# Performance work log

Hardware: AMD Instinct MI355X
Metric: run time of the kernel (lower is better)

Reference implementation:

```python
import jax, jax.numpy as jnp
import numpy as np
import math

D_SINGLE, D_PAIR, H, PQ, PV = 384, 128, 12, 4, 8
DH = D_SINGLE // H
OUT_DIM = H * DH + H * PV * 4 + H * D_PAIR


def setup_inputs() -> dict:
    key = jax.random.key(0)
    ks = jax.random.split(key, 24)
    B, L = 1, 512
    inp = {
        'single': jax.random.normal(ks[0], (B, L, D_SINGLE), jnp.float32),
        'pair': jax.random.normal(ks[1], (B, L, L, D_PAIR), jnp.float32),
        'rot_mats': jax.random.normal(ks[2], (B, L, 3, 3), jnp.float32),
        'trans': jax.random.normal(ks[3], (B, L, 3), jnp.float32),
        'mask': jnp.ones((B, L), jnp.float32),
        'ln_w': jnp.ones((D_SINGLE,), jnp.float32),
        'ln_b': jnp.zeros((D_SINGLE,), jnp.float32),
        'Wq': jax.random.normal(ks[4], (D_SINGLE, H * DH), jnp.float32) * 0.02,
        'bq': jnp.zeros((H * DH,), jnp.float32),
        'Wk': jax.random.normal(ks[5], (D_SINGLE, H * DH), jnp.float32) * 0.02,
        'bk': jnp.zeros((H * DH,), jnp.float32),
        'Wv': jax.random.normal(ks[6], (D_SINGLE, H * DH), jnp.float32) * 0.02,
        'bv': jnp.zeros((H * DH,), jnp.float32),
        'Wqp': jax.random.normal(ks[7], (D_SINGLE, H * PQ * 3), jnp.float32) * 0.02,
        'bqp': jnp.zeros((H * PQ * 3,), jnp.float32),
        'Wkp': jax.random.normal(ks[8], (D_SINGLE, H * PQ * 3), jnp.float32) * 0.02,
        'bkp': jnp.zeros((H * PQ * 3,), jnp.float32),
        'Wvp': jax.random.normal(ks[9], (D_SINGLE, H * PV * 3), jnp.float32) * 0.02,
        'bvp': jnp.zeros((H * PV * 3,), jnp.float32),
        'Wpb': jax.random.normal(ks[10], (D_PAIR, H), jnp.float32) * 0.02,
        'bpb': jnp.zeros((H,), jnp.float32),
        'Wo': jax.random.normal(ks[11], (OUT_DIM, D_SINGLE), jnp.float32) * 0.02,
        'bo': jnp.zeros((D_SINGLE,), jnp.float32),
        'w_c': jnp.asarray(1.0 / math.sqrt(3.0), jnp.float32),
        'w_l': jnp.asarray(1.0 / 3.0, jnp.float32),
        'gamma_h': jnp.ones((H,), jnp.float32),
    }
    return inp


def _layer_norm(x, w, b, eps=1e-5):
    mu = jnp.mean(x, axis=-1, keepdims=True)
    var = jnp.mean((x - mu) ** 2, axis=-1, keepdims=True)
    return (x - mu) * jax.lax.rsqrt(var + eps) * w + b


def reference(single, pair, rot_mats, trans, mask, ln_w, ln_b, Wq, bq, Wk, bk, Wv, bv,
              Wqp, bqp, Wkp, bkp, Wvp, bvp, Wpb, bpb, Wo, bo, w_c, w_l, gamma_h):
    B, L, _ = single.shape
    sn = _layer_norm(single, ln_w, ln_b)
    q = (sn @ Wq + bq).reshape(B, L, H, DH)
    k = (sn @ Wk + bk).reshape(B, L, H, DH)
    v = (sn @ Wv + bv).reshape(B, L, H, DH)
    qp = (sn @ Wqp + bqp).reshape(B, L, H, PQ, 3)
    kp = (sn @ Wkp + bkp).reshape(B, L, H, PQ, 3)
    vp = (sn @ Wvp + bvp).reshape(B, L, H, PV, 3)

    t = trans[:, :, None, None, :]  # [B,L,1,1,3]
    qg = jnp.einsum('blij,blhpj->blhpi', rot_mats, qp) + t
    kg = jnp.einsum('blij,blhpj->blhpi', rot_mats, kp) + t
    vg = jnp.einsum('blij,blhpj->blhpi', rot_mats, vp) + t

    # sequence logits [B,H,L,L]
    seq_logits = jnp.einsum('bihd,bjhd->bhij', q, k) * w_c / math.sqrt(DH)

    # geometric logits: pairwise point distances [B,H,L,L]
    q_pts = jnp.transpose(qg, (0, 2, 1, 3, 4))  # [B,H,L,PQ,3]
    k_pts = jnp.transpose(kg, (0, 2, 1, 3, 4))
    diff = q_pts[:, :, :, None] - k_pts[:, :, None]  # [B,H,L,L,PQ,3]
    dist_sq = jnp.sum(diff ** 2, axis=-1)            # [B,H,L,L,PQ]
    geo_logits = -0.5 * jnp.sum(dist_sq, axis=-1) * gamma_h[None, :, None, None] * w_l

    pair_bias = jnp.transpose(pair @ Wpb + bpb, (0, 3, 1, 2))  # [B,H,L,L]
    logits = seq_logits + geo_logits + pair_bias

    mask_2d = (mask[:, :, None] * mask[:, None, :])[:, None]  # [B,1,L,L]
    logits = jnp.where(mask_2d > 0, logits, jnp.float32(-1e9))
    attn = jax.nn.softmax(logits, axis=-1)  # [B,H,L,L]

    # sequence aggregation -> [B,L,H,DH]
    seq_out = jnp.einsum('bhij,bjhd->bihd', attn, v).reshape(B, L, H * DH)

    # point aggregation -> local frame features
    pts_out = jnp.einsum('bhij,bjhpd->bihpd', attn, vg)  # [B,L,H,PV,3]
    pts_local = jnp.einsum('blji,blhpj->blhpi', rot_mats, pts_out - t)
    pts_norm = jnp.linalg.norm(pts_local, axis=-1, keepdims=True)
    pts_feat = jnp.concatenate([pts_norm, pts_local], axis=-1).reshape(B, L, H * PV * 4)

    # pair aggregation -> [B,L,H*D_PAIR]
    pair_out = jnp.einsum('bhij,bijd->bihd', attn, pair).reshape(B, L, H * D_PAIR)

    combined = jnp.concatenate([seq_out, pts_feat, pair_out], axis=-1)
    return combined @ Wo + bo
```

## Files before the change

### kernel.cpp

```cpp
#include <hip/hip_runtime.h>
#include <math.h>

#define LQ    512
#define DS    384
#define DPAIR 128
#define NH    12
#define NPP   1792
#define FE2   64
#define TJC   64
#define NC    8

typedef unsigned short u16;
typedef unsigned int   u32;
typedef __attribute__((ext_vector_type(8))) short bf16x8;
typedef __attribute__((ext_vector_type(4))) float f32x4;

__device__ inline u16 bf16_rne(float x) {
  u32 u = __float_as_uint(x);
  u32 r = (u + 0x7FFFu + ((u >> 16) & 1u)) >> 16;
  return (u16)r;
}
__device__ inline void split_bf16(float x, u16& h, u16& l) {
  u16 hb = bf16_rne(x);
  float hf = __uint_as_float(((u32)hb) << 16);
  h = hb;
  l = bf16_rne(x - hf);
}

__global__ __launch_bounds__(256) void k_prep(
    const float* __restrict__ Wq, const float* __restrict__ Wk,
    const float* __restrict__ Wv, const float* __restrict__ Wqp,
    const float* __restrict__ Wkp, const float* __restrict__ Wvp,
    const float* __restrict__ bq, const float* __restrict__ bk,
    const float* __restrict__ bv, const float* __restrict__ bqp,
    const float* __restrict__ bkp, const float* __restrict__ bvp,
    const float* __restrict__ Wpb, const float* __restrict__ Wo,
    const float* __restrict__ xs, const float* __restrict__ ln_w,
    const float* __restrict__ ln_b,
    u16* __restrict__ Wth, u16* __restrict__ Wtl,
    float* __restrict__ bcat, float* __restrict__ WpbT,
    u16* __restrict__ WoTh, u16* __restrict__ WoTl,
    u16* __restrict__ snh, u16* __restrict__ snl) {
  __shared__ u16 sh_hi[64][66], sh_lo[64][66];
  int blk = blockIdx.x, t = threadIdx.x;
  if (blk < 168) {
    int kb = blk / 28, cb = blk % 28;
    int k0 = kb * 64, c0 = cb * 64;
    for (int e = t; e < 4096; e += 256) {
      int rr = e >> 6, cc = e & 63;
      int k = k0 + rr, c = c0 + cc;
      float v = 0.f;
      if (c < 384)       v = Wq[k*384 + c];
      else if (c < 768)  v = Wk[k*384 + c-384];
      else if (c < 1152) v = Wv[k*384 + c-768];
      else if (c < 1296) v = Wqp[k*144 + c-1152];
      else if (c < 1440) v = Wkp[k*144 + c-1296];
      else if (c < 1728) v = Wvp[k*288 + c-1440];
      u16 h_, l_; split_bf16(v, h_, l_);
      sh_hi[rr][cc] = h_; sh_lo[rr][cc] = l_;
    }
    __syncthreads();
// ... 91 lines not shown
    bf16x8 B1h = *(const bf16x8*)(b1h + k);
    bf16x8 A0l = *(const bf16x8*)(a0l + k);
    bf16x8 A1l = *(const bf16x8*)(a1l + k);
    bf16x8 B0l = *(const bf16x8*)(b0l + k);
    bf16x8 B1l = *(const bf16x8*)(b1l + k);
    c00 = __builtin_amdgcn_mfma_f32_16x16x32_bf16(A0h, B0h, c00, 0, 0, 0);
    c01 = __builtin_amdgcn_mfma_f32_16x16x32_bf16(A0h, B1h, c01, 0, 0, 0);
    c10 = __builtin_amdgcn_mfma_f32_16x16x32_bf16(A1h, B0h, c10, 0, 0, 0);
    c11 = __builtin_amdgcn_mfma_f32_16x16x32_bf16(A1h, B1h, c11, 0, 0, 0);
    c00 = __builtin_amdgcn_mfma_f32_16x16x32_bf16(A0h, B0l, c00, 0, 0, 0);
    c01 = __builtin_amdgcn_mfma_f32_16x16x32_bf16(A0h, B1l, c01, 0, 0, 0);
    c10 = __builtin_amdgcn_mfma_f32_16x16x32_bf16(A1h, B0l, c10, 0, 0, 0);
    c11 = __builtin_amdgcn_mfma_f32_16x16x32_bf16(A1h, B1l, c11, 0, 0, 0);
    c00 = __builtin_amdgcn_mfma_f32_16x16x32_bf16(A0l, B0h, c00, 0, 0, 0);
    c01 = __builtin_amdgcn_mfma_f32_16x16x32_bf16(A0l, B1h, c01, 0, 0, 0);
    c10 = __builtin_amdgcn_mfma_f32_16x16x32_bf16(A1l, B0h, c10, 0, 0, 0);
    c11 = __builtin_amdgcn_mfma_f32_16x16x32_bf16(A1l, B1h, c11, 0, 0, 0);
  }

  int orow = (lane >> 4) << 2;
  int col0 = j0 + lr, col1 = j0 + 16 + lr;
  if (KS == 1) {
    float bb0 = bias[col0], bb1 = bias[col1];
    #pragma unroll
    for (int r = 0; r < 4; r++) {
      int row0 = i0 + orow + r, row1 = row0 + 16;
      C[(size_t)row0*N + col0] = c00[r] + bb0;
      C[(size_t)row0*N + col1] = c01[r] + bb1;
      C[(size_t)row1*N + col0] = c10[r] + bb0;
      C[(size_t)row1*N + col1] = c11[r] + bb1;
    }
  } else {
    float* dst = Cpart + (size_t)blockIdx.z * M * N;
    #pragma unroll
    for (int r = 0; r < 4; r++) {
      int row0 = i0 + orow + r, row1 = row0 + 16;
      dst[(size_t)row0*N + col0] = c00[r];
      dst[(size_t)row0*N + col1] = c01[r];
      dst[(size_t)row1*N + col0] = c10[r];
      dst[(size_t)row1*N + col1] = c11[r];
    }
  }
}

__global__ void k_reduce_bias(const float* __restrict__ part, const float* __restrict__ bias,
                              float* __restrict__ out, int MN, int N, int KS) {
  int e = blockIdx.x * 256 + threadIdx.x;
  if (e >= MN) return;
  float s = bias[e % N];
  for (int z = 0; z < KS; z++) s += part[(size_t)z*MN + e];
  out[e] = s;
}

__global__ void k_rotfeat(const float* __restrict__ C1, const float* __restrict__ rot,
                          const float* __restrict__ trans, const float* __restrict__ gamma,
                          const float* __restrict__ w_c, const float* __restrict__ w_l,
                          u16* __restrict__ Afh, u16* __restrict__ Afl,
                          u16* __restrict__ Bfh, u16* __restrict__ Bfl,
                          u16* __restrict__ Vth, u16* __restrict__ Vtl) {
  int idx = blockIdx.x * 256 + threadIdx.x;
  if (idx >= LQ*NH) return;
  int h = idx % NH, i = idx / NH;
  float R[9], tr[3];
  #pragma unroll
  for (int r = 0; r < 9; r++) R[r] = rot[(size_t)i*9 + r];
  #pragma unroll
  for (int r = 0; r < 3; r++) tr[r] = trans[(size_t)i*3 + r];

  float s  = w_c[0] * rsqrtf(32.f);
  float gp = gamma[h] * w_l[0];
  size_t ab = ((size_t)h*LQ + i)*FE2;
  const float* q = C1 + (size_t)i*NPP + h*32;
  const float* k = C1 + (size_t)i*NPP + 384 + h*32;
  u16 h_, l_;
  #pragma unroll 8
  for (int d = 0; d < 32; d++) {
    split_bf16(s*q[d], h_, l_); Afh[ab+d] = h_; Afl[ab+d] = l_;
    split_bf16(k[d],   h_, l_); Bfh[ab+d] = h_; Bfl[ab+d] = l_;
  }

  const float* qp = C1 + (size_t)i*NPP + 1152 + h*12;
  const float* kp = C1 + (size_t)i*NPP + 1296 + h*12;
  float sq = 0.f, sk = 0.f;
  #pragma unroll
  for (int p = 0; p < 4; p++) {
    float x = qp[p*3], y = qp[p*3+1], z = qp[p*3+2];
    #pragma unroll
    for (int r = 0; r < 3; r++) {
      float g = fmaf(R[r*3],x, fmaf(R[r*3+1],y, fmaf(R[r*3+2],z, tr[r])));
      split_bf16(gp*g, h_, l_); Afh[ab+32+p*3+r] = h_; Afl[ab+32+p*3+r] = l_;
      sq = fmaf(g,g,sq);
    }
    float xk = kp[p*3], yk = kp[p*3+1], zk = kp[p*3+2];
    #pragma unroll
    for (int r = 0; r < 3; r++) {
      float g = fmaf(R[r*3],xk, fmaf(R[r*3+1],yk, fmaf(R[r*3+2],zk, tr[r])));
      split_bf16(g, h_, l_); Bfh[ab+32+p*3+r] = h_; Bfl[ab+32+p*3+r] = l_;
      sk = fmaf(g,g,sk);
    }
  }
  split_bf16(-0.5f*gp*sq, h_, l_); Afh[ab+44] = h_; Afl[ab+44] = l_;
  split_bf16(1.f, h_, l_);         Afh[ab+45] = h_; Afl[ab+45] = l_;
  split_bf16(1.f, h_, l_);         Bfh[ab+44] = h_; Bfl[ab+44] = l_;
  split_bf16(-0.5f*gp*sk, h_, l_); Bfh[ab+45] = h_; Bfl[ab+45] = l_;
  #pragma unroll
  for (int d = 46; d < FE2; d++) {
    Afh[ab+d] = 0; Afl[ab+d] = 0; Bfh[ab+d] = 0; Bfl[ab+d] = 0;
  }

  const float* vp = C1 + (size_t)i*NPP + 1440 + h*24;
  #pragma unroll 8
  for (int n = 0; n < 32; n++) {
    split_bf16(C1[(size_t)i*NPP + 768 + h*32 + n], h_, l_);
    Vth[((size_t)h*64 + n)*LQ + i] = h_; Vtl[((size_t)h*64 + n)*LQ + i] = l_;
  }
  #pragma unroll
  for (int p = 0; p < 8; p++) {
    float x = vp[p*3], y = vp[p*3+1], z = vp[p*3+2];
    #pragma unroll
    for (int r = 0; r < 3; r++) {
      float g = fmaf(R[r*3],x, fmaf(R[r*3+1],y, fmaf(R[r*3+2],z, tr[r])));
      split_bf16(g, h_, l_);
      Vth[((size_t)h*64 + 32 + p*3 + r)*LQ + i] = h_;
      Vtl[((size_t)h*64 + 32 + p*3 + r)*LQ + i] = l_;
    }
  }
  #pragma unroll
  for (int n = 56; n < 64; n++) {
    Vth[((size_t)h*64 + n)*LQ + i] = 0; Vtl[((size_t)h*64 + n)*LQ + i] = 0;
  }
}

__global__ __launch_bounds__(256) void k_logits_mfma(
    const u16* __restrict__ Afh, const u16* __restrict__ Afl,
    const u16* __restrict__ Bfh, const u16* __restrict__ Bfl,
    float* __restrict__ S) {
  int t = threadIdx.x;
  int lane = t & 63, wave = t >> 6;
  int wr = wave >> 1, wc = wave & 1;
  int h = blockIdx.z;
  int i0 = blockIdx.y * 64 + wr * 32;
  int j0 = blockIdx.x * 64 + wc * 32;
  int lr = lane & 15, lk = (lane >> 4) << 3;

  const u16* a0h = Afh + ((size_t)h*LQ + i0 + lr)*FE2 + lk;
  const u16* a1h = a0h + (size_t)16*FE2;
  const u16* a0l = Afl + ((size_t)h*LQ + i0 + lr)*FE2 + lk;
  const u16* a1l = a0l + (size_t)16*FE2;
  const u16* b0h = Bfh + ((size_t)h*LQ + j0 + lr)*FE2 + lk;
  const u16* b1h = b0h + (size_t)16*FE2;
  const u16* b0l = Bfl + ((size_t)h*LQ + j0 + lr)*FE2 + lk;
  const u16* b1l = b0l + (size_t)16*FE2;

  f32x4 c00 = {0.f,0.f,0.f,0.f}, c01 = c00, c10 = c00, c11 = c00;
  #pragma unroll
  for (int k = 0; k < FE2; k += 32) {
    bf16x8 A0h = *(const bf16x8*)(a0h + k);
    bf16x8 A1h = *(const bf16x8*)(a1h + k);
    bf16x8 B0h = *(const bf16x8*)(b0h + k);
    bf16x8 B1h = *(const bf16x8*)(b1h + k);
    bf16x8 A0l = *(const bf16x8*)(a0l + k);
    bf16x8 A1l = *(const bf16x8*)(a1l + k);
    bf16x8 B0l = *(const bf16x8*)(b0l + k);
    bf16x8 B1l = *(const bf16x8*)(b1l + k);
    c00 = __builtin_amdgcn_mfma_f32_16x16x32_bf16(A0h, B0h, c00, 0, 0, 0);
    c01 = __builtin_amdgcn_mfma_f32_16x16x32_bf16(A0h, B1h, c01, 0, 0, 0);
    c10 = __builtin_amdgcn_mfma_f32_16x16x32_bf16(A1h, B0h, c10, 0, 0, 0);
    c11 = __builtin_amdgcn_mfma_f32_16x16x32_bf16(A1h, B1h, c11, 0, 0, 0);
    c00 = __builtin_amdgcn_mfma_f32_16x16x32_bf16(A0h, B0l, c00, 0, 0, 0);
    c01 = __builtin_amdgcn_mfma_f32_16x16x32_bf16(A0h, B1l, c01, 0, 0, 0);
    c10 = __builtin_amdgcn_mfma_f32_16x16x32_bf16(A1h, B0l, c10, 0, 0, 0);
    c11 = __builtin_amdgcn_mfma_f32_16x16x32_bf16(A1h, B1l, c11, 0, 0, 0);
    c00 = __builtin_amdgcn_mfma_f32_16x16x32_bf16(A0l, B0h, c00, 0, 0, 0);
    c01 = __builtin_amdgcn_mfma_f32_16x16x32_bf16(A0l, B1h, c01, 0, 0, 0);
    c10 = __builtin_amdgcn_mfma_f32_16x16x32_bf16(A1l, B0h, c10, 0, 0, 0);
    c11 = __builtin_amdgcn_mfma_f32_16x16x32_bf16(A1l, B1h, c11, 0, 0, 0);
  }

  int orow = (lane >> 4) << 2;
  int col0 = j0 + lr, col1 = j0 + 16 + lr;
  #pragma unroll
  for (int r = 0; r < 4; r++) {
    int row0 = i0 + orow + r, row1 = row0 + 16;
    S[((size_t)h*LQ + row0)*LQ + col0] = c00[r];
    S[((size_t)h*LQ + row0)*LQ + col1] = c01[r];
    S[((size_t)h*LQ + row1)*LQ + col0] = c10[r];
    S[((size_t)h*LQ + row1)*LQ + col1] = c11[r];
  }
}

__global__ __launch_bounds__(256, 2) void k_pair_chunk(
    const float* __restrict__ pair, const float* __restrict__ WpbT,
    const float* __restrict__ bpb, const float* __restrict__ mask,
    float* __restrict__ S, float* __restrict__ pairpart, float* __restrict__ msum) {
  __shared__ float tile[TJC*133];
  __shared__ float wt[NH*TJC];
  int i = blockIdx.x, c = blockIdx.y, t = threadIdx.x;
  int j0 = c*TJC;

  const float4* src = (const float4*)(pair + ((size_t)i*LQ + j0)*DPAIR);
  #pragma unroll
  for (int u = 0; u < 8; u++) {
    int e = t + u*256; int row = e >> 5, c4 = e & 31;
    *(float4*)&tile[row*133 + c4*4] = src[e];
  }

  int j = t & 63;
  int hg = __builtin_amdgcn_readfirstlane(t >> 6);
  int h0 = hg*3;
  float l[3];
  #pragma unroll
  for (int q = 0; q < 3; q++)
    l[q] = S[((size_t)(h0+q)*LQ + i)*LQ + j0 + j] + bpb[h0+q];
  bool dead = (mask[i] * mask[j0 + j] <= 0.f);
  __syncthreads();

  {
    const float* w0p = WpbT + (size_t)(h0+0)*DPAIR;
    const float* w1p = WpbT + (size_t)(h0+1)*DPAIR;
    const float* w2p = WpbT + (size_t)(h0+2)*DPAIR;
    float a0 = 0.f, a1 = 0.f, a2 = 0.f;
    #pragma unroll 8
    for (int k = 0; k < DPAIR; k += 4) {
      float4 pv = *(const float4*)&tile[j*133 + k];
      float4 w0 = *(const float4*)(w0p + k);
      float4 w1 = *(const float4*)(w1p + k);
      float4 w2 = *(const float4*)(w2p + k);
      a0 = fmaf(pv.x,w0.x, fmaf(pv.y,w0.y, fmaf(pv.z,w0.z, fmaf(pv.w,w0.w, a0))));
      a1 = fmaf(pv.x,w1.x, fmaf(pv.y,w1.y, fmaf(pv.z,w1.z, fmaf(pv.w,w1.w, a1))));
      a2 = fmaf(pv.x,w2.x, fmaf(pv.y,w2.y, fmaf(pv.z,w2.z, fmaf(pv.w,w2.w, a2))));
    }
    l[0] += a0; l[1] += a1; l[2] += a2;
    if (dead) { l[0] = -1e9f; l[1] = -1e9f; l[2] = -1e9f; }
  }

  #pragma unroll
  for (int q = 0; q < 3; q++) {
    float m = l[q];
    #pragma unroll
    for (int o = 32; o > 0; o >>= 1) m = fmaxf(m, __shfl_xor(m, o, 64));
// ... 12 lines not shown

  int dg = t & 31, strip = t >> 5, jb = strip*8;
  float4 pv[8];
  #pragma unroll
  for (int q = 0; q < 8; q++) pv[q] = *(const float4*)&tile[(jb+q)*133 + dg*4];
  float4 acc[NH];
  #pragma unroll
  for (int h = 0; h < NH; h++) acc[h] = make_float4(0.f,0.f,0.f,0.f);
  #pragma unroll
  for (int h = 0; h < NH; h++) {
    float4 w0 = *(const float4*)&wt[h*TJC + jb];
    float4 w1 = *(const float4*)&wt[h*TJC + jb + 4];
    float wq[8] = {w0.x,w0.y,w0.z,w0.w,w1.x,w1.y,w1.z,w1.w};
    float4 a = acc[h];
    #pragma unroll
    for (int q = 0; q < 8; q++) {
      a.x = fmaf(wq[q], pv[q].x, a.x);
      a.y = fmaf(wq[q], pv[q].y, a.y);
      a.z = fmaf(wq[q], pv[q].z, a.z);
      a.w = fmaf(wq[q], pv[q].w, a.w);
    }
    acc[h] = a;
  }
  __syncthreads();

  float4* red4 = (float4*)tile;
  float4 tot[2];
  tot[0] = make_float4(0.f,0.f,0.f,0.f);
  tot[1] = make_float4(0.f,0.f,0.f,0.f);
  #pragma unroll
  for (int half = 0; half < 2; half++) {
    if ((strip >> 2) == half) {
      #pragma unroll
      for (int h = 0; h < NH; h++)
        red4[(((strip & 3)*NH) + h)*32 + dg] = acc[h];
    }
    __syncthreads();
    for (int e = t, u = 0; e < NH*32; e += 256, u++) {
      int rh = e >> 5, rd = e & 31;
      #pragma unroll
      for (int s4 = 0; s4 < 4; s4++) {
        float4 v = red4[((s4*NH) + rh)*32 + rd];
        tot[u].x += v.x; tot[u].y += v.y; tot[u].z += v.z; tot[u].w += v.w;
      }
    }
    __syncthreads();
  }
  for (int e = t, u = 0; e < NH*32; e += 256, u++) {
    int rh = e >> 5, rd = e & 31;
    *(float4*)&pairpart[(((size_t)i*NC + c)*NH + rh)*DPAIR + rd*4] = tot[u];
  }
}

__global__ __launch_bounds__(384) void k_scs_pairout(
    const float* __restrict__ msum, const float* __restrict__ pairpart,
    const float* __restrict__ S,
    u16* __restrict__ Awh, u16* __restrict__ Awl,
    u16* __restrict__ combh, u16* __restrict__ combl) {
  __shared__ float scs[NH*NC];
  int i = blockIdx.x, t = threadIdx.x;
  if (t < NH) {
    float m = -3.0e38f;
    float mc[NC], sc_[NC];
    #pragma unroll
    for (int c = 0; c < NC; c++) {
      const float* p = msum + (((size_t)i*NC + c)*NH + t)*2;
      mc[c] = p[0]; sc_[c] = p[1];
      m = fmaxf(m, mc[c]);
    }
    float s = 0.f;
    #pragma unroll
    for (int c = 0; c < NC; c++) s += sc_[c] * __expf(mc[c] - m);
    float inv = 1.f / s;
    #pragma unroll
    for (int c = 0; c < NC; c++)
      scs[t*NC + c] = __expf(mc[c] - m) * inv;
  }
  __syncthreads();
  int h = t >> 5, d = t & 31;
  float4 tot = make_float4(0.f,0.f,0.f,0.f);
  #pragma unroll
  for (int c = 0; c < NC; c++) {
    float sc = scs[h*NC + c];
    float4 v = *(const float4*)&pairpart[(((size_t)i*NC + c)*NH + h)*DPAIR + d*4];
    tot.x = fmaf(v.x, sc, tot.x); tot.y = fmaf(v.y, sc, tot.y);
    tot.z = fmaf(v.z, sc, tot.z); tot.w = fmaf(v.w, sc, tot.w);
  }
  size_t cb = (size_t)i*2304 + 768 + h*DPAIR + d*4;
  u16 h_, l_;
  split_bf16(tot.x, h_, l_); combh[cb+0] = h_; combl[cb+0] = l_;
  split_bf16(tot.y, h_, l_); combh[cb+1] = h_; combl[cb+1] = l_;
  split_bf16(tot.z, h_, l_); combh[cb+2] = h_; combl[cb+2] = l_;
  split_bf16(tot.w, h_, l_); combh[cb+3] = h_; combl[cb+3] = l_;
  for (int e = t; e < NH*LQ; e += 384) {
    int hh2 = e >> 9, j = e & 511;
    float w = S[((size_t)hh2*LQ + i)*LQ + j] * scs[hh2*NC + (j >> 6)];
    split_bf16(w, h_, l_);
    Awh[((size_t)hh2*LQ + i)*LQ + j] = h_;
    Awl[((size_t)hh2*LQ + i)*LQ + j] = l_;
  }
}

__global__ __launch_bounds__(256) void k_attn_mfma(
    const u16* __restrict__ Awh, const u16* __restrict__ Awl,
    const u16* __restrict__ Vth, const u16* __restrict__ Vtl,
    float* __restrict__ psum) {
  int t = threadIdx.x;
  int lane = t & 63, wave = t >> 6;
  int wr = wave >> 1, wc = wave & 1;
  int z = blockIdx.x;
  int i0 = blockIdx.y * 64 + wr * 32;
  int h = blockIdx.z;
  int n0 = wc * 32;
  int lr = lane & 15, lk = (lane >> 4) << 3;
  size_t kb = (size_t)z*128 + lk;

  const u16* a0h = Awh + ((size_t)h*LQ + i0 + lr)*LQ + kb;
  const u16* a1h = a0h + (size_t)16*LQ;
  const u16* a0l = Awl + ((size_t)h*LQ + i0 + lr)*LQ + kb;
  const u16* a1l = a0l + (size_t)16*LQ;
  const u16* b0h = Vth + ((size_t)h*64 + n0 + lr)*LQ + kb;
  const u16* b1h = b0h + (size_t)16*LQ;
  const u16* b0l = Vtl + ((size_t)h*64 + n0 + lr)*LQ + kb;
  const u16* b1l = b0l + (size_t)16*LQ;

  f32x4 c00 = {0.f,0.f,0.f,0.f}, c01 = c00, c10 = c00, c11 = c00;
  #pragma unroll
  for (int k = 0; k < 128; k += 32) {
    bf16x8 A0h = *(const bf16x8*)(a0h + k);
    bf16x8 A1h = *(const bf16x8*)(a1h + k);
    bf16x8 B0h = *(const bf16x8*)(b0h + k);
    bf16x8 B1h = *(const bf16x8*)(b1h + k);
    bf16x8 A0l = *(const bf16x8*)(a0l + k);
    bf16x8 A1l = *(const bf16x8*)(a1l + k);
    bf16x8 B0l = *(const bf16x8*)(b0l + k);
    bf16x8 B1l = *(const bf16x8*)(b1l + k);
    c00 = __builtin_amdgcn_mfma_f32_16x16x32_bf16(A0h, B0h, c00, 0, 0, 0);
    c01 = __builtin_amdgcn_mfma_f32_16x16x32_bf16(A0h, B1h, c01, 0, 0, 0);
    c10 = __builtin_amdgcn_mfma_f32_16x16x32_bf16(A1h, B0h, c10, 0, 0, 0);
    c11 = __builtin_amdgcn_mfma_f32_16x16x32_bf16(A1h, B1h, c11, 0, 0, 0);
    c00 = __builtin_amdgcn_mfma_f32_16x16x32_bf16(A0h, B0l, c00, 0, 0, 0);
    c01 = __builtin_amdgcn_mfma_f32_16x16x32_bf16(A0h, B1l, c01, 0, 0, 0);
    c10 = __builtin_amdgcn_mfma_f32_16x16x32_bf16(A1h, B0l, c10, 0, 0, 0);
    c11 = __builtin_amdgcn_mfma_f32_16x16x32_bf16(A1h, B1l, c11, 0, 0, 0);
    c00 = __builtin_amdgcn_mfma_f32_16x16x32_bf16(A0l, B0h, c00, 0, 0, 0);
    c01 = __builtin_amdgcn_mfma_f32_16x16x32_bf16(A0l, B1h, c01, 0, 0, 0);
    c10 = __builtin_amdgcn_mfma_f32_16x16x32_bf16(A1l, B0h, c10, 0, 0, 0);
    c11 = __builtin_amdgcn_mfma_f32_16x16x32_bf16(A1l, B1h, c11, 0, 0, 0);
  }

  int orow = (lane >> 4) << 2;
  int col0 = n0 + lr, col1 = n0 + 16 + lr;
  #pragma unroll
  for (int r = 0; r < 4; r++) {
    int row0 = i0 + orow + r, row1 = row0 + 16;
    psum[(((size_t)z*LQ + row0)*NH + h)*64 + col0] = c00[r];
    psum[(((size_t)z*LQ + row0)*NH + h)*64 + col1] = c01[r];
    psum[(((size_t)z*LQ + row1)*NH + h)*64 + col0] = c10[r];
    psum[(((size_t)z*LQ + row1)*NH + h)*64 + col1] = c11[r];
  }
}

__global__ void k_avpts(const float* __restrict__ psum, const float* __restrict__ rot,
                        const float* __restrict__ trans,
                        u16* __restrict__ combh, u16* __restrict__ combl) {
  int idx = blockIdx.x * 256 + threadIdx.x;
  if (idx >= LQ*NH*40) return;
  int w = idx % 40; int ih = idx / 40; int h = ih % NH; int i = ih / NH;
  size_t base = ((size_t)i*NH + h)*64;
  u16 h_, l_;
  if (w < 32) {
    float s = 0.f;
    for (int z = 0; z < 4; z++) s += psum[(size_t)z*LQ*NH*64 + base + w];
    split_bf16(s, h_, l_);
    combh[(size_t)i*2304 + h*32 + w] = h_;
    combl[(size_t)i*2304 + h*32 + w] = l_;
  } else {
    int p = w - 32;
    float g[3];
    #pragma unroll
    for (int r = 0; r < 3; r++) {
      int n = 32 + p*3 + r;
      float s = 0.f;
      for (int z = 0; z < 4; z++) s += psum[(size_t)z*LQ*NH*64 + base + n];
      g[r] = s;
    }
    const float* R = rot + (size_t)i*9;
    const float* tr = trans + (size_t)i*3;
    float x = g[0]-tr[0], y = g[1]-tr[1], z = g[2]-tr[2];
    float lx = fmaf(R[0],x, fmaf(R[3],y, R[6]*z));
    float ly = fmaf(R[1],x, fmaf(R[4],y, R[7]*z));
    float lz = fmaf(R[2],x, fmaf(R[5],y, R[8]*z));
    float nrm = sqrtf(fmaf(lx,lx, fmaf(ly,ly, lz*lz)));
    size_t dst = (size_t)i*2304 + 384 + (h*8 + p)*4;
    split_bf16(nrm, h_, l_); combh[dst+0] = h_; combl[dst+0] = l_;
    split_bf16(lx,  h_, l_); combh[dst+1] = h_; combl[dst+1] = l_;
    split_bf16(ly,  h_, l_); combh[dst+2] = h_; combl[dst+2] = l_;
    split_bf16(lz,  h_, l_); combh[dst+3] = h_; combl[dst+3] = l_;
  }
}

extern "C" void kernel_launch(void* const* d_in, const int* in_sizes, int n_in,
                              void* d_out, int out_size, void* d_ws, size_t ws_size,
                              hipStream_t stream) {
  const float* single = (const float*)d_in[0];
  const float* pair   = (const float*)d_in[1];
  const float* rot    = (const float*)d_in[2];
  const float* trans  = (const float*)d_in[3];
  const float* mask   = (const float*)d_in[4];
  const float* ln_w   = (const float*)d_in[5];
  const float* ln_b   = (const float*)d_in[6];
  const float* Wq     = (const float*)d_in[7];
  const float* bq     = (const float*)d_in[8];
  const float* Wk     = (const float*)d_in[9];
  const float* bk     = (const float*)d_in[10];
  const float* Wv     = (const float*)d_in[11];
  const float* bv     = (const float*)d_in[12];
  const float* Wqp    = (const float*)d_in[13];
  const float* bqp    = (const float*)d_in[14];
  const float* Wkp    = (const float*)d_in[15];
  const float* bkp    = (const float*)d_in[16];
  const float* Wvp    = (const float*)d_in[17];
  const float* bvp    = (const float*)d_in[18];
  const float* Wpb    = (const float*)d_in[19];
  const float* bpb    = (const float*)d_in[20];
  const float* Wo     = (const float*)d_in[21];
  const float* bo     = (const float*)d_in[22];
  const float* w_c    = (const float*)d_in[23];
  const float* w_l    = (const float*)d_in[24];
  const float* gamma  = (const float*)d_in[25];
  float* out = (float*)d_out;

  float* p = (float*)d_ws;
  auto alloc = [&](size_t n) { float* r = p; p += n; return r; };
  u16* WcatTh = (u16*)alloc((size_t)NPP*DS/2);
  u16* WcatTl = (u16*)alloc((size_t)NPP*DS/2);
  u16* snh    = (u16*)alloc((size_t)LQ*DS/2);
  u16* snl    = (u16*)alloc((size_t)LQ*DS/2);
  u16* WoTh   = (u16*)alloc((size_t)DS*2304/2);
  u16* WoTl   = (u16*)alloc((size_t)DS*2304/2);
  u16* combh  = (u16*)alloc((size_t)LQ*2304/2);
  u16* combl  = (u16*)alloc((size_t)LQ*2304/2);
  u16* Afh    = (u16*)alloc((size_t)NH*LQ*FE2/2);
  u16* Afl    = (u16*)alloc((size_t)NH*LQ*FE2/2);
  u16* Bfh    = (u16*)alloc((size_t)NH*LQ*FE2/2);
  u16* Bfl    = (u16*)alloc((size_t)NH*LQ*FE2/2);
  u16* Vth    = (u16*)alloc((size_t)NH*64*LQ/2);
  u16* Vtl    = (u16*)alloc((size_t)NH*64*LQ/2);
  u16* Awh    = (u16*)alloc((size_t)NH*LQ*LQ/2);
  u16* Awl    = (u16*)alloc((size_t)NH*LQ*LQ/2);
  float* bcat    = alloc(NPP);
  float* WpbT    = alloc((size_t)NH*DPAIR);
  float* C1      = alloc((size_t)LQ*NPP);
  float* S       = alloc((size_t)NH*LQ*LQ);
  float* pairpart= alloc((size_t)LQ*NC*NH*DPAIR);
  float* msum    = alloc((size_t)LQ*NC*NH*2);
  float* psum    = alloc((size_t)4*LQ*NH*64);
  float* outpart = alloc((size_t)8*LQ*DS);

  k_prep<<<dim3(897), 256, 0, stream>>>(
      Wq, Wk, Wv, Wqp, Wkp, Wvp, bq, bk, bv, bqp, bkp, bvp, Wpb, Wo,
      single, ln_w, ln_b, WcatTh, WcatTl, bcat, WpbT, WoTh, WoTl, snh, snl);
  k_gemm_mfma<<<dim3(NPP/64, LQ/64, 1), 256, 0, stream>>>(
      snh, snl, WcatTh, WcatTl, bcat, C1, nullptr, LQ, NPP, DS);
  k_rotfeat<<<dim3((LQ*NH + 255)/256), 256, 0, stream>>>(
      C1, rot, trans, gamma, w_c, w_l, Afh, Afl, Bfh, Bfl, Vth, Vtl);
  k_logits_mfma<<<dim3(LQ/64, LQ/64, NH), 256, 0, stream>>>(Afh, Afl, Bfh, Bfl, S);
  k_pair_chunk<<<dim3(LQ, NC), 256, 0, stream>>>(pair, WpbT, bpb, mask, S, pairpart, msum);
  k_scs_pairout<<<dim3(LQ), 384, 0, stream>>>(msum, pairpart, S, Awh, Awl, combh, combl);
  k_attn_mfma<<<dim3(4, LQ/64, NH), 256, 0, stream>>>(Awh, Awl, Vth, Vtl, psum);
  k_avpts<<<dim3((LQ*NH*40 + 255)/256), 256, 0, stream>>>(psum, rot, trans, combh, combl);
  k_gemm_mfma<<<dim3(DS/64, LQ/64, 8), 256, 0, stream>>>(
      combh, combl, WoTh, WoTl, nullptr, nullptr, outpart, LQ, DS, 2304);
  k_reduce_bias<<<dim3((LQ*DS + 255)/256), 256, 0, stream>>>(outpart, bo, out, LQ*DS, DS, 8);
}
```

Baseline: 366.3 us.

## Fuse feature prep into logits and fuse softmax-scale, AV and point output

Feature building (rotated query/key points, bf16 hi/lo split) moves into the logits kernel, which builds its 64-row tiles in shared memory. The score rescale, attention-times-value MFMA, pair-output reduction and point back-rotation are merged into one per-(row block, head) kernel. This removes the large intermediate bf16 attention-weight and feature buffers, the psum buffer, and three launches. In exchange, features are recomputed for every tile, and the fused attention kernel runs only 96 blocks, each looping over the key dimension, so parallelism drops sharply.

Result: slower. 373.8 us (+2.1%).

```diff
diff --git a/kernel.cpp b/kernel.cpp
--- a/kernel.cpp
+++ b/kernel.cpp
@@ -6,7 +6,6 @@
 #define DPAIR 128
 #define NH    12
 #define NPP   1792
-#define FE2   64
 #define TJC   64
 #define NC    8
 
@@ -204,117 +203,70 @@
   out[e] = s;
 }
 
-__global__ void k_rotfeat(const float* __restrict__ C1, const float* __restrict__ rot,
-                          const float* __restrict__ trans, const float* __restrict__ gamma,
-                          const float* __restrict__ w_c, const float* __restrict__ w_l,
-                          u16* __restrict__ Afh, u16* __restrict__ Afl,
-                          u16* __restrict__ Bfh, u16* __restrict__ Bfl,
-                          u16* __restrict__ Vth, u16* __restrict__ Vtl) {
-  int idx = blockIdx.x * 256 + threadIdx.x;
-  if (idx >= LQ*NH) return;
-  int h = idx % NH, i = idx / NH;
-  float R[9], tr[3];
-  #pragma unroll
-  for (int r = 0; r < 9; r++) R[r] = rot[(size_t)i*9 + r];
-  #pragma unroll
-  for (int r = 0; r < 3; r++) tr[r] = trans[(size_t)i*3 + r];
-
-  float s  = w_c[0] * rsqrtf(32.f);
-  float gp = gamma[h] * w_l[0];
-  size_t ab = ((size_t)h*LQ + i)*FE2;
-  const float* q = C1 + (size_t)i*NPP + h*32;
-  const float* k = C1 + (size_t)i*NPP + 384 + h*32;
-  u16 h_, l_;
-  #pragma unroll 8
-  for (int d = 0; d < 32; d++) {
-    split_bf16(s*q[d], h_, l_); Afh[ab+d] = h_; Afl[ab+d] = l_;
-    split_bf16(k[d],   h_, l_); Bfh[ab+d] = h_; Bfl[ab+d] = l_;
-  }
-
-  const float* qp = C1 + (size_t)i*NPP + 1152 + h*12;
-  const float* kp = C1 + (size_t)i*NPP + 1296 + h*12;
-  float sq = 0.f, sk = 0.f;
-  #pragma unroll
-  for (int p = 0; p < 4; p++) {
-    float x = qp[p*3], y = qp[p*3+1], z = qp[p*3+2];
-    #pragma unroll
-    for (int r = 0; r < 3; r++) {
-      float g = fmaf(R[r*3],x, fmaf(R[r*3+1],y, fmaf(R[r*3+2],z, tr[r])));
-      split_bf16(gp*g, h_, l_); Afh[ab+32+p*3+r] = h_; Afl[ab+32+p*3+r] = l_;
-      sq = fmaf(g,g,sq);
-    }
-    float xk = kp[p*3], yk = kp[p*3+1], zk = kp[p*3+2];
-    #pragma unroll
-    for (int r = 0; r < 3; r++) {
-      float g = fmaf(R[r*3],xk, fmaf(R[r*3+1],yk, fmaf(R[r*3+2],zk, tr[r])));
-      split_bf16(g, h_, l_); Bfh[ab+32+p*3+r] = h_; Bfl[ab+32+p*3+r] = l_;
-      sk = fmaf(g,g,sk);
-    }
-  }
-  split_bf16(-0.5f*gp*sq, h_, l_); Afh[ab+44] = h_; Afl[ab+44] = l_;
-  split_bf16(1.f, h_, l_);         Afh[ab+45] = h_; Afl[ab+45] = l_;
-  split_bf16(1.f, h_, l_);         Bfh[ab+44] = h_; Bfl[ab+44] = l_;
-  split_bf16(-0.5f*gp*sk, h_, l_); Bfh[ab+45] = h_; Bfl[ab+45] = l_;
-  #pragma unroll
-  for (int d = 46; d < FE2; d++) {
-    Afh[ab+d] = 0; Afl[ab+d] = 0; Bfh[ab+d] = 0; Bfl[ab+d] = 0;
-  }
-
-  const float* vp = C1 + (size_t)i*NPP + 1440 + h*24;
-  #pragma unroll 8
-  for (int n = 0; n < 32; n++) {
-    split_bf16(C1[(size_t)i*NPP + 768 + h*32 + n], h_, l_);
-    Vth[((size_t)h*64 + n)*LQ + i] = h_; Vtl[((size_t)h*64 + n)*LQ + i] = l_;
-  }
-  #pragma unroll
-  for (int p = 0; p < 8; p++) {
-    float x = vp[p*3], y = vp[p*3+1], z = vp[p*3+2];
-    #pragma unroll
-    for (int r = 0; r < 3; r++) {
-      float g = fmaf(R[r*3],x, fmaf(R[r*3+1],y, fmaf(R[r*3+2],z, tr[r])));
-      split_bf16(g, h_, l_);
-      Vth[((size_t)h*64 + 32 + p*3 + r)*LQ + i] = h_;
-      Vtl[((size_t)h*64 + 32 + p*3 + r)*LQ + i] = l_;
-    }
-  }
-  #pragma unroll
-  for (int n = 56; n < 64; n++) {
-    Vth[((size_t)h*64 + n)*LQ + i] = 0; Vtl[((size_t)h*64 + n)*LQ + i] = 0;
-  }
-}
-
-__global__ __launch_bounds__(256) void k_logits_mfma(
-    const u16* __restrict__ Afh, const u16* __restrict__ Afl,
-    const u16* __restrict__ Bfh, const u16* __restrict__ Bfl,
+__global__ __launch_bounds__(256) void k_feat_logits(
+    const float* __restrict__ C1, const float* __restrict__ rot,
+    const float* __restrict__ trans, const float* __restrict__ gamma,
+    const float* __restrict__ w_c, const float* __restrict__ w_l,
     float* __restrict__ S) {
+  __shared__ u16 Ash[64][72], Asl[64][72], Bsh[64][72], Bsl[64][72];
+  int h = blockIdx.z;
+  int i0 = blockIdx.y * 64, j0 = blockIdx.x * 64;
   int t = threadIdx.x;
-  int lane = t & 63, wave = t >> 6;
-  int wr = wave >> 1, wc = wave & 1;
-  int h = blockIdx.z;
-  int i0 = blockIdx.y * 64 + wr * 32;
-  int j0 = blockIdx.x * 64 + wc * 32;
+
+  if (t < 128) {
+    int row = t & 63, side = t >> 6;
+    int gi = (side ? j0 : i0) + row;
+    float R[9], tr[3];
+    #pragma unroll
+    for (int r = 0; r < 9; r++) R[r] = rot[(size_t)gi*9 + r];
+    #pragma unroll
+    for (int r = 0; r < 3; r++) tr[r] = trans[(size_t)gi*3 + r];
+    float sc = w_c[0] * rsqrtf(32.f);
+    float gp = gamma[h] * w_l[0];
+    u16 (*Fh)[72] = side ? Bsh : Ash;
+    u16 (*Fl)[72] = side ? Bsl : Asl;
+    const float* qk = C1 + (size_t)gi*NPP + (side ? 384 : 0) + h*32;
+    u16 h_, l_;
+    #pragma unroll 8
+    for (int d = 0; d < 32; d++) {
+      float v = side ? qk[d] : sc*qk[d];
+      split_bf16(v, h_, l_); Fh[row][d] = h_; Fl[row][d] = l_;
+    }
+    const float* pp = C1 + (size_t)gi*NPP + (side ? 1296 : 1152) + h*12;
+    float ss = 0.f;
+    #pragma unroll
+    for (int p = 0; p < 4; p++) {
+      float x = pp[p*3], y = pp[p*3+1], z = pp[p*3+2];
+      #pragma unroll
+      for (int r = 0; r < 3; r++) {
+        float g = fmaf(R[r*3],x, fmaf(R[r*3+1],y, fmaf(R[r*3+2],z, tr[r])));
+        float v = side ? g : gp*g;
+        split_bf16(v, h_, l_); Fh[row][32+p*3+r] = h_; Fl[row][32+p*3+r] = l_;
+        ss = fmaf(g,g,ss);
+      }
+    }
+    float c44 = side ? 1.f : -0.5f*gp*ss;
+    float c45 = side ? -0.5f*gp*ss : 1.f;
+    split_bf16(c44, h_, l_); Fh[row][44] = h_; Fl[row][44] = l_;
+    split_bf16(c45, h_, l_); Fh[row][45] = h_; Fl[row][45] = l_;
+    #pragma unroll
+    for (int d = 46; d < 64; d++) { Fh[row][d] = 0; Fl[row][d] = 0; }
+  }
+  __syncthreads();
+
+  int lane = t & 63, wave = t >> 6, wr = wave >> 1, wc = wave & 1;
   int lr = lane & 15, lk = (lane >> 4) << 3;
-
-  const u16* a0h = Afh + ((size_t)h*LQ + i0 + lr)*FE2 + lk;
-  const u16* a1h = a0h + (size_t)16*FE2;
-  const u16* a0l = Afl + ((size_t)h*LQ + i0 + lr)*FE2 + lk;
-  const u16* a1l = a0l + (size_t)16*FE2;
-  const u16* b0h = Bfh + ((size_t)h*LQ + j0 + lr)*FE2 + lk;
-  const u16* b1h = b0h + (size_t)16*FE2;
-  const u16* b0l = Bfl + ((size_t)h*LQ + j0 + lr)*FE2 + lk;
-  const u16* b1l = b0l + (size_t)16*FE2;
-
   f32x4 c00 = {0.f,0.f,0.f,0.f}, c01 = c00, c10 = c00, c11 = c00;
   #pragma unroll
-  for (int k = 0; k < FE2; k += 32) {
-    bf16x8 A0h = *(const bf16x8*)(a0h + k);
-    bf16x8 A1h = *(const bf16x8*)(a1h + k);
-    bf16x8 B0h = *(const bf16x8*)(b0h + k);
-    bf16x8 B1h = *(const bf16x8*)(b1h + k);
-    bf16x8 A0l = *(const bf16x8*)(a0l + k);
-    bf16x8 A1l = *(const bf16x8*)(a1l + k);
-    bf16x8 B0l = *(const bf16x8*)(b0l + k);
-    bf16x8 B1l = *(const bf16x8*)(b1l + k);
+  for (int ks = 0; ks < 64; ks += 32) {
+    bf16x8 A0h = *(const bf16x8*)&Ash[wr*32 + lr][ks + lk];
+    bf16x8 A1h = *(const bf16x8*)&Ash[wr*32 + 16 + lr][ks + lk];
+    bf16x8 B0h = *(const bf16x8*)&Bsh[wc*32 + lr][ks + lk];
+    bf16x8 B1h = *(const bf16x8*)&Bsh[wc*32 + 16 + lr][ks + lk];
+    bf16x8 A0l = *(const bf16x8*)&Asl[wr*32 + lr][ks + lk];
+    bf16x8 A1l = *(const bf16x8*)&Asl[wr*32 + 16 + lr][ks + lk];
+    bf16x8 B0l = *(const bf16x8*)&Bsl[wc*32 + lr][ks + lk];
+    bf16x8 B1l = *(const bf16x8*)&Bsl[wc*32 + 16 + lr][ks + lk];
     c00 = __builtin_amdgcn_mfma_f32_16x16x32_bf16(A0h, B0h, c00, 0, 0, 0);
     c01 = __builtin_amdgcn_mfma_f32_16x16x32_bf16(A0h, B1h, c01, 0, 0, 0);
     c10 = __builtin_amdgcn_mfma_f32_16x16x32_bf16(A1h, B0h, c10, 0, 0, 0);
@@ -330,14 +282,14 @@
   }
 
   int orow = (lane >> 4) << 2;
-  int col0 = j0 + lr, col1 = j0 + 16 + lr;
+  int col0 = j0 + wc*32 + lr, col1 = col0 + 16;
+  int rbase = i0 + wr*32 + orow;
   #pragma unroll
   for (int r = 0; r < 4; r++) {
-    int row0 = i0 + orow + r, row1 = row0 + 16;
-    S[((size_t)h*LQ + row0)*LQ + col0] = c00[r];
-    S[((size_t)h*LQ + row0)*LQ + col1] = c01[r];
-    S[((size_t)h*LQ + row1)*LQ + col0] = c10[r];
-    S[((size_t)h*LQ + row1)*LQ + col1] = c11[r];
+    S[((size_t)h*LQ + rbase + r)*LQ + col0]      = c00[r];
+    S[((size_t)h*LQ + rbase + r)*LQ + col1]      = c01[r];
+    S[((size_t)h*LQ + rbase + 16 + r)*LQ + col0] = c10[r];
+    S[((size_t)h*LQ + rbase + 16 + r)*LQ + col1] = c11[r];
   }
 }
 
@@ -456,151 +408,149 @@
   }
 }
 
-__global__ __launch_bounds__(384) void k_scs_pairout(
-    const float* __restrict__ msum, const float* __restrict__ pairpart,
-    const float* __restrict__ S,
-    u16* __restrict__ Awh, u16* __restrict__ Awl,
+__global__ __launch_bounds__(256, 2) void k_attn_full(
+    const float* __restrict__ S, const float* __restrict__ msum,
+    const float* __restrict__ pairpart,
+    const float* __restrict__ C1, const float* __restrict__ rot,
+    const float* __restrict__ trans,
     u16* __restrict__ combh, u16* __restrict__ combl) {
-  __shared__ float scs[NH*NC];
-  int i = blockIdx.x, t = threadIdx.x;
-  if (t < NH) {
-    float m = -3.0e38f;
-    float mc[NC], sc_[NC];
+  __shared__ u16 Ash[64][72], Asl[64][72], Vsh[64][72], Vsl[64][72];
+  __shared__ float scs_l[64][NC];
+  __shared__ float Of[64][66];
+  int i0 = blockIdx.x * 64;
+  int h = blockIdx.y;
+  int t = threadIdx.x, lane = t & 63, wave = t >> 6, wr = wave >> 1, wc = wave & 1;
+  int lr = lane & 15, lk = (lane >> 4) << 3;
+
+  if (t < 64) {
+    int gi = i0 + t;
+    float mc[NC], sc[NC], m = -3.0e38f;
     #pragma unroll
     for (int c = 0; c < NC; c++) {
-      const float* p = msum + (((size_t)i*NC + c)*NH + t)*2;
-      mc[c] = p[0]; sc_[c] = p[1];
+      const float* p = msum + (((size_t)gi*NC + c)*NH + h)*2;
+      mc[c] = p[0]; sc[c] = p[1];
       m = fmaxf(m, mc[c]);
     }
+    float den = 0.f;
+    #pragma unroll
+    for (int c = 0; c < NC; c++) den += sc[c] * __expf(mc[c] - m);
+    float inv = 1.f / den;
+    #pragma unroll
+    for (int c = 0; c < NC; c++) scs_l[t][c] = __expf(mc[c] - m) * inv;
+  }
+  __syncthreads();
+
+  for (int e = t; e < 64*DPAIR; e += 256) {
+    int m = e >> 7, d = e & 127;
     float s = 0.f;
     #pragma unroll
-    for (int c = 0; c < NC; c++) s += sc_[c] * __expf(mc[c] - m);
-    float inv = 1.f / s;
-    #pragma unroll
     for (int c = 0; c < NC; c++)
-      scs[t*NC + c] = __expf(mc[c] - m) * inv;
+      s = fmaf(scs_l[m][c], pairpart[(((size_t)(i0+m)*NC + c)*NH + h)*DPAIR + d], s);
+    u16 h_, l_; split_bf16(s, h_, l_);
+    size_t dst = (size_t)(i0+m)*2304 + 768 + h*DPAIR + d;
+    combh[dst] = h_; combl[dst] = l_;
+  }
+
+  f32x4 c00 = {0.f,0.f,0.f,0.f}, c01 = c00, c10 = c00, c11 = c00;
+  for (int jc = 0; jc < 8; jc++) {
+    int j0 = jc * 64;
+    for (int e = t; e < 4096; e += 256) {
+      int m = e >> 6, j = e & 63;
+      float w = S[((size_t)h*LQ + i0 + m)*LQ + j0 + j] * scs_l[m][jc];
+      u16 h_, l_; split_bf16(w, h_, l_);
+      Ash[m][j] = h_; Asl[m][j] = l_;
+    }
+    {
+      int j = t & 63, ng = t >> 6;
+      int gj = j0 + j;
+      u16 h_, l_;
+      if (ng < 2) {
+        const float* vrow = C1 + (size_t)gj*NPP + 768 + h*32 + ng*16;
+        #pragma unroll
+        for (int q = 0; q < 16; q++) {
+          split_bf16(vrow[q], h_, l_);
+          Vsh[ng*16 + q][j] = h_; Vsl[ng*16 + q][j] = l_;
+        }
+      } else {
+        const float* prow = C1 + (size_t)gj*NPP + 1440 + h*24;
+        const float* R = rot + (size_t)gj*9;
+        const float* tr = trans + (size_t)gj*3;
+        int nbase = ng * 16;
+        #pragma unroll
+        for (int q = 0; q < 16; q++) {
+          int n = nbase + q;
+          float val = 0.f;
+          if (n < 56) {
+            int pp = (n - 32) / 3, rr = (n - 32) % 3;
+            float x = prow[pp*3], y = prow[pp*3+1], z = prow[pp*3+2];
+            val = fmaf(R[rr*3], x, fmaf(R[rr*3+1], y, fmaf(R[rr*3+2], z, tr[rr])));
+          }
+          split_bf16(val, h_, l_);
+          Vsh[n][j] = h_; Vsl[n][j] = l_;
+        }
+      }
+    }
+    __syncthreads();
+    #pragma unroll
+    for (int ks = 0; ks < 64; ks += 32) {
+      bf16x8 A0h = *(const bf16x8*)&Ash[wr*32 + lr][ks + lk];
+      bf16x8 A1h = *(const bf16x8*)&Ash[wr*32 + 16 + lr][ks + lk];
+      bf16x8 B0h = *(const bf16x8*)&Vsh[wc*32 + lr][ks + lk];
+      bf16x8 B1h = *(const bf16x8*)&Vsh[wc*32 + 16 + lr][ks + lk];
+      bf16x8 A0l = *(const bf16x8*)&Asl[wr*32 + lr][ks + lk];
+      bf16x8 A1l = *(const bf16x8*)&Asl[wr*32 + 16 + lr][ks + lk];
+      bf16x8 B0l = *(const bf16x8*)&Vsl[wc*32 + lr][ks + lk];
+      bf16x8 B1l = *(const bf16x8*)&Vsl[wc*32 + 16 + lr][ks + lk];
+      c00 = __builtin_amdgcn_mfma_f32_16x16x32_bf16(A0h, B0h, c00, 0, 0, 0);
+      c01 = __builtin_amdgcn_mfma_f32_16x16x32_bf16(A0h, B1h, c01, 0, 0, 0);
+      c10 = __builtin_amdgcn_mfma_f32_16x16x32_bf16(A1h, B0h, c10, 0, 0, 0);
+      c11 = __builtin_amdgcn_mfma_f32_16x16x32_bf16(A1h, B1h, c11, 0, 0, 0);
+      c00 = __builtin_amdgcn_mfma_f32_16x16x32_bf16(A0h, B0l, c00, 0, 0, 0);
+      c01 = __builtin_amdgcn_mfma_f32_16x16x32_bf16(A0h, B1l, c01, 0, 0, 0);
+      c10 = __builtin_amdgcn_mfma_f32_16x16x32_bf16(A1h, B0l, c10, 0, 0, 0);
+      c11 = __builtin_amdgcn_mfma_f32_16x16x32_bf16(A1h, B1l, c11, 0, 0, 0);
+      c00 = __builtin_amdgcn_mfma_f32_16x16x32_bf16(A0l, B0h, c00, 0, 0, 0);
+      c01 = __builtin_amdgcn_mfma_f32_16x16x32_bf16(A0l, B1h, c01, 0, 0, 0);
+      c10 = __builtin_amdgcn_mfma_f32_16x16x32_bf16(A1l, B0h, c10, 0, 0, 0);
+      c11 = __builtin_amdgcn_mfma_f32_16x16x32_bf16(A1l, B1h, c11, 0, 0, 0);
+    }
+    __syncthreads();
+  }
+
+  int orow = (lane >> 4) << 2;
+  #pragma unroll
+  for (int r = 0; r < 4; r++) {
+    Of[wr*32 + orow + r][wc*32 + lr]           = c00[r];
+    Of[wr*32 + orow + r][wc*32 + 16 + lr]      = c01[r];
+    Of[wr*32 + 16 + orow + r][wc*32 + lr]      = c10[r];
+    Of[wr*32 + 16 + orow + r][wc*32 + 16 + lr] = c11[r];
   }
   __syncthreads();
-  int h = t >> 5, d = t & 31;
-  float4 tot = make_float4(0.f,0.f,0.f,0.f);
-  #pragma unroll
-  for (int c = 0; c < NC; c++) {
-    float sc = scs[h*NC + c];
-    float4 v = *(const float4*)&pairpart[(((size_t)i*NC + c)*NH + h)*DPAIR + d*4];
-    tot.x = fmaf(v.x, sc, tot.x); tot.y = fmaf(v.y, sc, tot.y);
-    tot.z = fmaf(v.z, sc, tot.z); tot.w = fmaf(v.w, sc, tot.w);
-  }
-  size_t cb = (size_t)i*2304 + 768 + h*DPAIR + d*4;
-  u16 h_, l_;
-  split_bf16(tot.x, h_, l_); combh[cb+0] = h_; combl[cb+0] = l_;
-  split_bf16(tot.y, h_, l_); combh[cb+1] = h_; combl[cb+1] = l_;
-  split_bf16(tot.z, h_, l_); combh[cb+2] = h_; combl[cb+2] = l_;
-  split_bf16(tot.w, h_, l_); combh[cb+3] = h_; combl[cb+3] = l_;
-  for (int e = t; e < NH*LQ; e += 384) {
-    int hh2 = e >> 9, j = e & 511;
-    float w = S[((size_t)hh2*LQ + i)*LQ + j] * scs[hh2*NC + (j >> 6)];
-    split_bf16(w, h_, l_);
-    Awh[((size_t)hh2*LQ + i)*LQ + j] = h_;
-    Awl[((size_t)hh2*LQ + i)*LQ + j] = l_;
-  }
-}
-
-__global__ __launch_bounds__(256) void k_attn_mfma(
-    const u16* __restrict__ Awh, const u16* __restrict__ Awl,
-    const u16* __restrict__ Vth, const u16* __restrict__ Vtl,
-    float* __restrict__ psum) {
-  int t = threadIdx.x;
-  int lane = t & 63, wave = t >> 6;
-  int wr = wave >> 1, wc = wave & 1;
-  int z = blockIdx.x;
-  int i0 = blockIdx.y * 64 + wr * 32;
-  int h = blockIdx.z;
-  int n0 = wc * 32;
-  int lr = lane & 15, lk = (lane >> 4) << 3;
-  size_t kb = (size_t)z*128 + lk;
-
-  const u16* a0h = Awh + ((size_t)h*LQ + i0 + lr)*LQ + kb;
-  const u16* a1h = a0h + (size_t)16*LQ;
-  const u16* a0l = Awl + ((size_t)h*LQ + i0 + lr)*LQ + kb;
-  const u16* a1l = a0l + (size_t)16*LQ;
-  const u16* b0h = Vth + ((size_t)h*64 + n0 + lr)*LQ + kb;
-  const u16* b1h = b0h + (size_t)16*LQ;
-  const u16* b0l = Vtl + ((size_t)h*64 + n0 + lr)*LQ + kb;
-  const u16* b1l = b0l + (size_t)16*LQ;
-
-  f32x4 c00 = {0.f,0.f,0.f,0.f}, c01 = c00, c10 = c00, c11 = c00;
-  #pragma unroll
-  for (int k = 0; k < 128; k += 32) {
-    bf16x8 A0h = *(const bf16x8*)(a0h + k);
-    bf16x8 A1h = *(const bf16x8*)(a1h + k);
-    bf16x8 B0h = *(const bf16x8*)(b0h + k);
-    bf16x8 B1h = *(const bf16x8*)(b1h + k);
-    bf16x8 A0l = *(const bf16x8*)(a0l + k);
-    bf16x8 A1l = *(const bf16x8*)(a1l + k);
-    bf16x8 B0l = *(const bf16x8*)(b0l + k);
-    bf16x8 B1l = *(const bf16x8*)(b1l + k);
-    c00 = __builtin_amdgcn_mfma_f32_16x16x32_bf16(A0h, B0h, c00, 0, 0, 0);
-    c01 = __builtin_amdgcn_mfma_f32_16x16x32_bf16(A0h, B1h, c01, 0, 0, 0);
-    c10 = __builtin_amdgcn_mfma_f32_16x16x32_bf16(A1h, B0h, c10, 0, 0, 0);
-    c11 = __builtin_amdgcn_mfma_f32_16x16x32_bf16(A1h, B1h, c11, 0, 0, 0);
-    c00 = __builtin_amdgcn_mfma_f32_16x16x32_bf16(A0h, B0l, c00, 0, 0, 0);
-    c01 = __builtin_amdgcn_mfma_f32_16x16x32_bf16(A0h, B1l, c01, 0, 0, 0);
-    c10 = __builtin_amdgcn_mfma_f32_16x16x32_bf16(A1h, B0l, c10, 0, 0, 0);
-    c11 = __builtin_amdgcn_mfma_f32_16x16x32_bf16(A1h, B1l, c11, 0, 0, 0);
-    c00 = __builtin_amdgcn_mfma_f32_16x16x32_bf16(A0l, B0h, c00, 0, 0, 0);
-    c01 = __builtin_amdgcn_mfma_f32_16x16x32_bf16(A0l, B1h, c01, 0, 0, 0);
-    c10 = __builtin_amdgcn_mfma_f32_16x16x32_bf16(A1l, B0h, c10, 0, 0, 0);
-    c11 = __builtin_amdgcn_mfma_f32_16x16x32_bf16(A1l, B1h, c11, 0, 0, 0);
-  }
-
-  int orow = (lane >> 4) << 2;
-  int col0 = n0 + lr, col1 = n0 + 16 + lr;
-  #pragma unroll
-  for (int r = 0; r < 4; r++) {
-    int row0 = i0 + orow + r, row1 = row0 + 16;
-    psum[(((size_t)z*LQ + row0)*NH + h)*64 + col0] = c00[r];
-    psum[(((size_t)z*LQ + row0)*NH + h)*64 + col1] = c01[r];
-    psum[(((size_t)z*LQ + row1)*NH + h)*64 + col0] = c10[r];
-    psum[(((size_t)z*LQ + row1)*NH + h)*64 + col1] = c11[r];
-  }
-}
-
-__global__ void k_avpts(const float* __restrict__ psum, const float* __restrict__ rot,
-                        const float* __restrict__ trans,
-                        u16* __restrict__ combh, u16* __restrict__ combl) {
-  int idx = blockIdx.x * 256 + threadIdx.x;
-  if (idx >= LQ*NH*40) return;
-  int w = idx % 40; int ih = idx / 40; int h = ih % NH; int i = ih / NH;
-  size_t base = ((size_t)i*NH + h)*64;
-  u16 h_, l_;
-  if (w < 32) {
-    float s = 0.f;
-    for (int z = 0; z < 4; z++) s += psum[(size_t)z*LQ*NH*64 + base + w];
-    split_bf16(s, h_, l_);
-    combh[(size_t)i*2304 + h*32 + w] = h_;
-    combl[(size_t)i*2304 + h*32 + w] = l_;
-  } else {
-    int p = w - 32;
-    float g[3];
-    #pragma unroll
-    for (int r = 0; r < 3; r++) {
-      int n = 32 + p*3 + r;
-      float s = 0.f;
-      for (int z = 0; z < 4; z++) s += psum[(size_t)z*LQ*NH*64 + base + n];
-      g[r] = s;
-    }
-    const float* R = rot + (size_t)i*9;
-    const float* tr = trans + (size_t)i*3;
-    float x = g[0]-tr[0], y = g[1]-tr[1], z = g[2]-tr[2];
-    float lx = fmaf(R[0],x, fmaf(R[3],y, R[6]*z));
-    float ly = fmaf(R[1],x, fmaf(R[4],y, R[7]*z));
-    float lz = fmaf(R[2],x, fmaf(R[5],y, R[8]*z));
-    float nrm = sqrtf(fmaf(lx,lx, fmaf(ly,ly, lz*lz)));
-    size_t dst = (size_t)i*2304 + 384 + (h*8 + p)*4;
-    split_bf16(nrm, h_, l_); combh[dst+0] = h_; combl[dst+0] = l_;
-    split_bf16(lx,  h_, l_); combh[dst+1] = h_; combl[dst+1] = l_;
-    split_bf16(ly,  h_, l_); combh[dst+2] = h_; combl[dst+2] = l_;
-    split_bf16(lz,  h_, l_); combh[dst+3] = h_; combl[dst+3] = l_;
+
+  for (int e = t; e < 64*40; e += 256) {
+    int w = e % 40, m = e / 40;
+    int gi = i0 + m;
+    u16 h_, l_;
+    if (w < 32) {
+      split_bf16(Of[m][w], h_, l_);
+      combh[(size_t)gi*2304 + h*32 + w] = h_;
+      combl[(size_t)gi*2304 + h*32 + w] = l_;
+    } else {
+      int pp = w - 32;
+      float g0 = Of[m][32+pp*3], g1 = Of[m][32+pp*3+1], g2 = Of[m][32+pp*3+2];
+      const float* R = rot + (size_t)gi*9;
+      const float* tr = trans + (size_t)gi*3;
+      float x = g0 - tr[0], y = g1 - tr[1], z = g2 - tr[2];
+      float lx = fmaf(R[0],x, fmaf(R[3],y, R[6]*z));
+      float ly = fmaf(R[1],x, fmaf(R[4],y, R[7]*z));
+      float lz = fmaf(R[2],x, fmaf(R[5],y, R[8]*z));
+      float nrm = sqrtf(fmaf(lx,lx, fmaf(ly,ly, lz*lz)));
+      size_t dst = (size_t)gi*2304 + 384 + ((size_t)h*8 + pp)*4;
+      split_bf16(nrm, h_, l_); combh[dst+0] = h_; combl[dst+0] = l_;
+      split_bf16(lx,  h_, l_); combh[dst+1] = h_; combl[dst+1] = l_;
+      split_bf16(ly,  h_, l_); combh[dst+2] = h_; combl[dst+2] = l_;
+      split_bf16(lz,  h_, l_); combh[dst+3] = h_; combl[dst+3] = l_;
+    }
   }
 }
 
@@ -645,21 +595,12 @@
   u16* WoTl   = (u16*)alloc((size_t)DS*2304/2);
   u16* combh  = (u16*)alloc((size_t)LQ*2304/2);
   u16* combl  = (u16*)alloc((size_t)LQ*2304/2);
-  u16* Afh    = (u16*)alloc((size_t)NH*LQ*FE2/2);
-  u16* Afl    = (u16*)alloc((size_t)NH*LQ*FE2/2);
-  u16* Bfh    = (u16*)alloc((size_t)NH*LQ*FE2/2);
-  u16* Bfl    = (u16*)alloc((size_t)NH*LQ*FE2/2);
-  u16* Vth    = (u16*)alloc((size_t)NH*64*LQ/2);
-  u16* Vtl    = (u16*)alloc((size_t)NH*64*LQ/2);
-  u16* Awh    = (u16*)alloc((size_t)NH*LQ*LQ/2);
-  u16* Awl    = (u16*)alloc((size_t)NH*LQ*LQ/2);
   float* bcat    = alloc(NPP);
   float* WpbT    = alloc((size_t)NH*DPAIR);
   float* C1      = alloc((size_t)LQ*NPP);
   float* S       = alloc((size_t)NH*LQ*LQ);
   float* pairpart= alloc((size_t)LQ*NC*NH*DPAIR);
   float* msum    = alloc((size_t)LQ*NC*NH*2);
-  float* psum    = alloc((size_t)4*LQ*NH*64);
   float* outpart = alloc((size_t)8*LQ*DS);
 
   k_prep<<<dim3(897), 256, 0, stream>>>(
@@ -667,13 +608,11 @@
       single, ln_w, ln_b, WcatTh, WcatTl, bcat, WpbT, WoTh, WoTl, snh, snl);
   k_gemm_mfma<<<dim3(NPP/64, LQ/64, 1), 256, 0, stream>>>(
       snh, snl, WcatTh, WcatTl, bcat, C1, nullptr, LQ, NPP, DS);
-  k_rotfeat<<<dim3((LQ*NH + 255)/256), 256, 0, stream>>>(
-      C1, rot, trans, gamma, w_c, w_l, Afh, Afl, Bfh, Bfl, Vth, Vtl);
-  k_logits_mfma<<<dim3(LQ/64, LQ/64, NH), 256, 0, stream>>>(Afh, Afl, Bfh, Bfl, S);
+  k_feat_logits<<<dim3(LQ/64, LQ/64, NH), 256, 0, stream>>>(
+      C1, rot, trans, gamma, w_c, w_l, S);
   k_pair_chunk<<<dim3(LQ, NC), 256, 0, stream>>>(pair, WpbT, bpb, mask, S, pairpart, msum);
-  k_scs_pairout<<<dim3(LQ), 384, 0, stream>>>(msum, pairpart, S, Awh, Awl, combh, combl);
-  k_attn_mfma<<<dim3(4, LQ/64, NH), 256, 0, stream>>>(Awh, Awl, Vth, Vtl, psum);
-  k_avpts<<<dim3((LQ*NH*40 + 255)/256), 256, 0, stream>>>(psum, rot, trans, combh, combl);
+  k_attn_full<<<dim3(LQ/64, NH), 256, 0, stream>>>(
+      S, msum, pairpart, C1, rot, trans, combh, combl);
   k_gemm_mfma<<<dim3(DS/64, LQ/64, 8), 256, 0, stream>>>(
       combh, combl, WoTh, WoTl, nullptr, nullptr, outpart, LQ, DS, 2304);
   k_reduce_bias<<<dim3((LQ*DS + 255)/256), 256, 0, stream>>>(outpart, bo, out, LQ*DS, DS, 8);
```
